# Performance work log

Measured on AMD Instinct MI355X. Metric: run time of the kernel, lower is better.

Reference implementation:

```python
import jax, jax.numpy as jnp
import numpy as np

N_ROUTING = 3


def squash(s):
    # squash factor ||s|| / (1 + ||s||^2), applied per output capsule vector
    n = jnp.linalg.norm(s, axis=-1, keepdims=True)
    return n / (1.0 + n * n) * s


def setup_inputs() -> dict:
    key = jax.random.key(0)
    k1, k2 = jax.random.split(key)
    B, Ni, Di = 64, 2048, 8
    No, Do = 32, 16
    x = jax.random.normal(k1, (B, Ni, Di), dtype=jnp.float32)
    W = jax.random.normal(k2, (Ni, No, Do, Di), dtype=jnp.float32) * 0.05
    return {"x": x, "W": W}


def reference(x, W):
    # x: (B, Ni, Di); W: (Ni, No, Do, Di)
    # Per-capsule transform: x_hat[b,i,j,:] = W[i,j] @ x[b,i]
    x_hat = jnp.einsum('bni,nodi->bnod', x, W)          # (B, Ni, No, Do)
    x_hat_sg = jax.lax.stop_gradient(x_hat)
    B, Ni, No, Do = x_hat.shape
    b = jnp.zeros((B, Ni, No), dtype=x_hat.dtype)       # routing logits
    v = None
    for it in range(N_ROUTING):
        c = jax.nn.softmax(b, axis=2)                   # coupling over output caps
        if it == N_ROUTING - 1:
            s = jnp.einsum('bno,bnod->bod', c, x_hat)   # grads flow on last iter
            v = squash(s)
        else:
            s = jnp.einsum('bno,bnod->bod', c, x_hat_sg)
            v = squash(s)
            b = b + jnp.einsum('bod,bnod->bno', v, x_hat_sg)  # agreement update
    return v  # (B, No, Do)
```

## Files before the change

kernel.cpp:

```cpp
#include <hip/hip_runtime.h>
#include <hip/hip_bf16.h>
#include <math.h>

namespace {
constexpr int kB  = 64;
constexpr int kNi = 2048;
constexpr int kNo = 32;
constexpr int kDo = 16;
constexpr int kSeg   = kNo * kDo;
constexpr int kSlabs = 256;
constexpr int kNPer  = kNi / kSlabs;
}

typedef __attribute__((ext_vector_type(4)))  short s4;
typedef __attribute__((ext_vector_type(16))) float f16v;

__device__ __forceinline__ f16v mfma_32x32x8_bf16(s4 a, s4 b, f16v c) {
#if __has_builtin(__builtin_amdgcn_mfma_f32_32x32x8bf16_1k)
    return __builtin_amdgcn_mfma_f32_32x32x8bf16_1k(a, b, c, 0, 0, 0);
#else
    asm("v_mfma_f32_32x32x8_bf16 %0, %1, %2, %0" : "+v"(c) : "v"(a), "v"(b));
    return c;
#endif
}

__device__ __forceinline__ unsigned pack_bf16(float lo, float hi) {
    union { __hip_bfloat162 h; unsigned u; } v;
    v.h = __float22bfloat162_rn(make_float2(lo, hi));
    return v.u;
}
__device__ __forceinline__ float bf_lo(unsigned u) { return __uint_as_float(u << 16); }
__device__ __forceinline__ float bf_hi(unsigned u) { return __uint_as_float(u & 0xffff0000u); }

union A2 { int2 i; s4 s; };


__global__ __launch_bounds__(512, 2)
void caps_prepacc(const float* __restrict__ xg, const float* __restrict__ Wg,
                  unsigned* __restrict__ wPack2, unsigned* __restrict__ xPack,
                  __hip_bfloat16* __restrict__ partial)
{
    const int tid = threadIdx.x;
    const int blk = blockIdx.x;
    const int w   = __builtin_amdgcn_readfirstlane(tid >> 6);
    const int l   = tid & 63;
    const int o32 = l & 31;
    const int hi  = l >> 5;

    const float4* Wg4 = reinterpret_cast<const float4*>(Wg);
    const float4* xg4 = reinterpret_cast<const float4*>(xg);

    f16v acc00, acc01, acc10, acc11;
#pragma unroll
    for (int r = 0; r < 16; ++r) {
        acc00[r] = 0.0f; acc01[r] = 0.0f; acc10[r] = 0.0f; acc11[r] = 0.0f;
    }

#pragma unroll 2
    for (int nn = 0; nn < kNPer; ++nn) {
        const int n = blk * kNPer + nn;
        const float4 w0 = Wg4[((size_t)n * 512 + (2 * w + 0) * 32 + o32) * 2 + hi];
        const float4 w1 = Wg4[((size_t)n * 512 + (2 * w + 1) * 32 + o32) * 2 + hi];
        int4 wp;
        wp.x = (int)pack_bf16(w0.x, w0.y);
        wp.y = (int)pack_bf16(w0.z, w0.w);
        wp.z = (int)pack_bf16(w1.x, w1.y);
        wp.w = (int)pack_bf16(w1.z, w1.w);
        reinterpret_cast<int4*>(wPack2)[((size_t)n * 8 + w) * 64 + l] = wp;

        const float4 x0 = xg4[((size_t)(0 * 32 + o32) * kNi + n) * 2 + hi];
        const float4 x1 = xg4[((size_t)(32 + o32) * kNi + n) * 2 + hi];
        uint2 q0, q1;
        q0.x = pack_bf16(x0.x, x0.y); q0.y = pack_bf16(x0.z, x0.w);
        q1.x = pack_bf16(x1.x, x1.y); q1.y = pack_bf16(x1.z, x1.w);
        *reinterpret_cast<uint2*>(xPack + ((size_t)(n * 2 + 0) * 64 + l) * 2) = q0;
        *reinterpret_cast<uint2*>(xPack + ((size_t)(n * 2 + 1) * 64 + l) * 2) = q1;

        A2 a0; a0.i = make_int2(wp.x, wp.y);
        A2 a1; a1.i = make_int2(wp.z, wp.w);
        A2 b0; b0.i = make_int2((int)q0.x, (int)q0.y);
        A2 b1; b1.i = make_int2((int)q1.x, (int)q1.y);
        acc00 = mfma_32x32x8_bf16(a0.s, b0.s, acc00);
        acc01 = mfma_32x32x8_bf16(a1.s, b0.s, acc01);
        acc10 = mfma_32x32x8_bf16(a0.s, b1.s, acc10);
        acc11 = mfma_32x32x8_bf16(a1.s, b1.s, acc11);
    }

#pragma unroll
    for (int nt = 0; nt < 2; ++nt) {
        const int b = nt * 32 + o32;
#pragma unroll
        for (int m = 0; m < 2; ++m) {
            const int mt = 2 * w + m;
            const f16v& a = (nt == 0) ? (m == 0 ? acc00 : acc01)
                                      : (m == 0 ? acc10 : acc11);
#pragma unroll
            for (int q = 0; q < 4; ++q) {
                const int od = mt * 32 + 8 * q + 4 * hi;
                uint2 u;
                u.x = pack_bf16(a[4 * q + 0], a[4 * q + 1]);
                u.y = pack_bf16(a[4 * q + 2], a[4 * q + 3]);
                *reinterpret_cast<uint2*>(
                    partial + ((size_t)blk * kB + b) * kSeg + od) = u;
            }
        }
    }
}

__global__ __launch_bounds__(512, 2)
void caps_routef(const unsigned* __restrict__ wPack2, const unsigned* __restrict__ xPack,
                 const float* __restrict__ vsumPack, __hip_bfloat16* __restrict__ partial)
{
    __shared__ float Zl[2][8][4][32];
    __shared__ unsigned cl[kNPer][16][32];

    const int tid = threadIdx.x;
    const int blk = blockIdx.x & (kSlabs - 1);
    const int nt  = blockIdx.x >> 8;
    const int w   = __builtin_amdgcn_readfirstlane(tid >> 6);
    const int l   = tid & 63;
    const int b32 = l & 31;
    const int b   = nt * 32 + b32;
    const int hi  = l >> 5;

    const int4* wp4 = reinterpret_cast<const int4*>(wPack2);
    const int2* xp2 = reinterpret_cast<const int2*>(xPack);
    const size_t abase = ((size_t)blk * 64 + w) * 64 + l;
    const size_t xbase = ((size_t)blk * 16 + nt) * 64 + l;

    {
        float vsp[2][16];
#pragma unroll
        for (int m = 0; m < 2; ++m) {
            const int mt = 2 * w + m;
            const float4* vp = reinterpret_cast<const float4*>(
                vsumPack + (((size_t)mt * 2 + hi) * 64 + b) * 16);
#pragma unroll
            for (int k = 0; k < 4; ++k) {
                const float4 v = vp[k];
                vsp[m][4 * k + 0] = v.x; vsp[m][4 * k + 1] = v.y;
                vsp[m][4 * k + 2] = v.z; vsp[m][4 * k + 3] = v.w;
            }
        }

        for (int h = 0; h < 2; ++h) {
            float e[4][4];
#pragma unroll
            for (int k = 0; k < 4; ++k) {
                const int nn = h * 4 + k;
                const int4 aw = wp4[abase + (size_t)nn * 512];
                const int2 bx = xp2[xbase + (size_t)nn * 128];
                A2 ua0; ua0.i = make_int2(aw.x, aw.y);
                A2 ua1; ua1.i = make_int2(aw.z, aw.w);
                A2 ub;  ub.i  = bx;
                f16v t0, t1;
#pragma unroll
                for (int r = 0; r < 16; ++r) { t0[r] = 0.0f; t1[r] = 0.0f; }
                t0 = mfma_32x32x8_bf16(ua0.s, ub.s, t0);
                t1 = mfma_32x32x8_bf16(ua1.s, ub.s, t1);
                {
                    float a0_ = fmaf(vsp[0][1], t0[1], vsp[0][0] * t0[0]);
                    float a1_ = fmaf(vsp[0][3], t0[3], vsp[0][2] * t0[2]);
                    float a2_ = fmaf(vsp[0][5], t0[5], vsp[0][4] * t0[4]);
                    float a3_ = fmaf(vsp[0][7], t0[7], vsp[0][6] * t0[6]);
                    float p0 = (a0_ + a1_) + (a2_ + a3_);
                    float b0_ = fmaf(vsp[0][9],  t0[9],  vsp[0][8]  * t0[8]);
                    float b1_ = fmaf(vsp[0][11], t0[11], vsp[0][10] * t0[10]);
                    float b2_ = fmaf(vsp[0][13], t0[13], vsp[0][12] * t0[12]);
                    float b3_ = fmaf(vsp[0][15], t0[15], vsp[0][14] * t0[14]);
                    float p1 = (b0_ + b1_) + (b2_ + b3_);
                    p0 += __shfl_xor(p0, 32);
                    p1 += __shfl_xor(p1, 32);
                    e[k][0] = exp2f(p0); e[k][1] = exp2f(p1);
                }
                {
                    float a0_ = fmaf(vsp[1][1], t1[1], vsp[1][0] * t1[0]);
                    float a1_ = fmaf(vsp[1][3], t1[3], vsp[1][2] * t1[2]);
                    float a2_ = fmaf(vsp[1][5], t1[5], vsp[1][4] * t1[4]);
                    float a3_ = fmaf(vsp[1][7], t1[7], vsp[1][6] * t1[6]);
                    float p0 = (a0_ + a1_) + (a2_ + a3_);
                    float b0_ = fmaf(vsp[1][9],  t1[9],  vsp[1][8]  * t1[8]);
                    float b1_ = fmaf(vsp[1][11], t1[11], vsp[1][10] * t1[10]);
                    float b2_ = fmaf(vsp[1][13], t1[13], vsp[1][12] * t1[12]);
                    float b3_ = fmaf(vsp[1][15], t1[15], vsp[1][14] * t1[14]);
                    float p1 = (b0_ + b1_) + (b2_ + b3_);
                    p0 += __shfl_xor(p0, 32);
                    p1 += __shfl_xor(p1, 32);
                    e[k][2] = exp2f(p0); e[k][3] = exp2f(p1);
                }
                if (l < 32)
                    Zl[h][w][k][l] = (e[k][0] + e[k][1]) + (e[k][2] + e[k][3]);
            }
            __syncthreads();
#pragma unroll
            for (int k = 0; k < 4; ++k) {
                float Z = 0.0f;
#pragma unroll
                for (int w2 = 0; w2 < 8; ++w2) Z += Zl[h][w2][k][b32];
                const float rz = __builtin_amdgcn_rcpf(Z);
                if (l < 32) {
                    cl[h * 4 + k][2 * w + 0][l] = pack_bf16(e[k][0] * rz, e[k][1] * rz);
                    cl[h * 4 + k][2 * w + 1][l] = pack_bf16(e[k][2] * rz, e[k][3] * rz);
                }
            }
        }
    }
    __syncthreads();
    __builtin_amdgcn_sched_barrier(0);

    float sacc[2][16];
#pragma unroll
    for (int r = 0; r < 16; ++r) { sacc[0][r] = 0.0f; sacc[1][r] = 0.0f; }

#pragma unroll 2
    for (int nn = 0; nn < kNPer; ++nn) {
        const int4 aw = wp4[abase + (size_t)nn * 512];
        const int2 bx = xp2[xbase + (size_t)nn * 128];
        A2 ua0; ua0.i = make_int2(aw.x, aw.y);
        A2 ua1; ua1.i = make_int2(aw.z, aw.w);
        A2 ub;  ub.i  = bx;
        const unsigned cp0 = cl[nn][2 * w + 0][b32];
        const unsigned cp1 = cl[nn][2 * w + 1][b32];
        f16v t0, t1;
#pragma unroll
        for (int r = 0; r < 16; ++r) { t0[r] = 0.0f; t1[r] = 0.0f; }
        t0 = mfma_32x32x8_bf16(ua0.s, ub.s, t0);
        t1 = mfma_32x32x8_bf16(ua1.s, ub.s, t1);
        const float c00 = bf_lo(cp0), c01 = bf_hi(cp0);
        const float c10 = bf_lo(cp1), c11 = bf_hi(cp1);
#pragma unroll
        for (int r = 0; r < 8; ++r) {
            sacc[0][r]     = fmaf(c00, t0[r],     sacc[0][r]);
            sacc[0][8 + r] = fmaf(c01, t0[8 + r], sacc[0][8 + r]);
            sacc[1][r]     = fmaf(c10, t1[r],     sacc[1][r]);
            sacc[1][8 + r] = fmaf(c11, t1[8 + r], sacc[1][8 + r]);
        }
    }

#pragma unroll
    for (int m = 0; m < 2; ++m) {
        const int mt = 2 * w + m;
#pragma unroll
        for (int q = 0; q < 4; ++q) {
            const int od = mt * 32 + 8 * q + 4 * hi;
            uint2 u;
            u.x = pack_bf16(sacc[m][4 * q + 0], sacc[m][4 * q + 1]);
            u.y = pack_bf16(sacc[m][4 * q + 2], sacc[m][4 * q + 3]);
            *reinterpret_cast<uint2*>(
                partial + ((size_t)blk * kB + b) * kSeg + od) = u;
        }
    }
}

template<int PASS>
__global__ __launch_bounds__(512, 2)
void caps_finish(const __hip_bfloat16* __restrict__ partial,
                 float* __restrict__ vsum, float* __restrict__ vsumPack,
                 float* __restrict__ out)
{
    const int b  = blockIdx.x >> 2;
    const int q  = blockIdx.x & 3;
    const int t  = threadIdx.x;
    const int qd = t & 31;
    const int sg = t >> 5;
    const int od0 = q * 128 + qd * 4;

    const __hip_bfloat16* p = partial
        + ((size_t)(sg * 16) * kB + b) * kSeg + od0;
    float s0 = 0, s1 = 0, s2 = 0, s3 = 0;
#pragma unroll
    for (int k = 0; k < 16; ++k) {
        const uint2 u = *reinterpret_cast<const uint2*>(p + (size_t)k * (kB * kSeg));
        s0 += bf_lo(u.x); s1 += bf_hi(u.x);
        s2 += bf_lo(u.y); s3 += bf_hi(u.y);
    }

    __shared__ float red[16][128];
    __shared__ float sq[128];
    __shared__ float fo[8];
    *reinterpret_cast<float4*>(&red[sg][qd * 4]) = make_float4(s0, s1, s2, s3);
    __syncthreads();
    if (t < 128) {
        float s = 0.0f;
#pragma unroll
        for (int g = 0; g < 16; ++g) s += red[g][t];
        if (PASS == 0) s *= (1.0f / 32.0f);
        sq[t] = s * s;
        red[0][t] = s;
    }
    __syncthreads();
    if (t < 8) {
        float n2 = 0.0f;
#pragma unroll
        for (int d = 0; d < 16; ++d) n2 += sq[t * 16 + d];
        fo[t] = sqrtf(n2) / (1.0f + n2);
    }
    __syncthreads();
    if (t < 128) {
        const float s = red[0][t];
        const int od = q * 128 + t;
        const float v = fo[t >> 4] * s;
        float nv = v;
        if (PASS == 0) {
            vsum[(size_t)b * kSeg + od] = v;
        } else if (PASS == 1) {
            nv = vsum[(size_t)b * kSeg + od] + v;
            vsum[(size_t)b * kSeg + od] = nv;
        } else {
            out[(size_t)b * kSeg + od] = v;
        }
        if (PASS < 2) {
            const int mt = od >> 5, r5 = od & 31;
            const int hi = (r5 >> 2) & 1, reg = (r5 & 3) | ((r5 >> 3) << 2);
            vsumPack[(((size_t)mt * 2 + hi) * 64 + b) * 16 + reg] =
                nv * 1.44269504f;
        }
    }
}

extern "C" void kernel_launch(void* const* d_in, const int* in_sizes, int n_in,
                              void* d_out, int out_size, void* d_ws, size_t ws_size,
                              hipStream_t stream)
{
    const float* x = (const float*)d_in[0];
    const float* W = (const float*)d_in[1];
    float* out = (float*)d_out;

    char* base = (char*)d_ws;
    __hip_bfloat16* partial = (__hip_bfloat16*)base;
    base += (size_t)kSlabs * kB * kSeg * sizeof(__hip_bfloat16);
    float* vsum = (float*)base;
    base += (size_t)kB * kSeg * sizeof(float);
    float* vsumPack = (float*)base;
    base += (size_t)16 * 2 * 64 * 16 * sizeof(float);
    unsigned* wPack2 = (unsigned*)base;
    base += (size_t)kNi * 16 * 64 * 2 * sizeof(unsigned);
    unsigned* xPack = (unsigned*)base;

    const dim3 gp(kSlabs), bp(512);
    const dim3 gr(kSlabs * 2), br(512);
    const dim3 gf(kB * 4), bf(512);

    caps_prepacc<<<gp, bp, 0, stream>>>(x, W, wPack2, xPack, partial);
    caps_finish<0><<<gf, bf, 0, stream>>>(partial, vsum, vsumPack, out);
    caps_routef<<<gr, br, 0, stream>>>(wPack2, xPack, vsumPack, partial);
    caps_finish<1><<<gf, bf, 0, stream>>>(partial, vsum, vsumPack, out);
    caps_routef<<<gr, br, 0, stream>>>(wPack2, xPack, vsumPack, partial);
    caps_finish<2><<<gf, bf, 0, stream>>>(partial, vsum, vsumPack, out);
}
```

Baseline: 71.87 us.

## Fuse all routing stages into one cooperative kernel with grid syncs

Merges the six launches (prep/accumulate, three finish passes, two routing passes) into one persistent cooperative kernel of 256 blocks, with grid-wide syncs between stages. The routing body now loops over both batch halves inside each block instead of using 512 blocks. This removes launch overhead and inter-kernel gaps, but halves routing parallelism, drops occupancy to one block per CU by launch bounds, and adds grid barrier costs.

Result: slower. 269.0 us (+274.3%).

```diff
diff --git a/kernel.cpp b/kernel.cpp
--- a/kernel.cpp
+++ b/kernel.cpp
@@ -1,13 +1,14 @@
 #include <hip/hip_runtime.h>
 #include <hip/hip_bf16.h>
+#include <hip/hip_cooperative_groups.h>
 #include <math.h>
+
+namespace cg = cooperative_groups;
 
 namespace {
 constexpr int kB  = 64;
 constexpr int kNi = 2048;
-constexpr int kNo = 32;
-constexpr int kDo = 16;
-constexpr int kSeg   = kNo * kDo;
+constexpr int kSeg   = 512;
 constexpr int kSlabs = 256;
 constexpr int kNPer  = kNi / kSlabs;
 }
@@ -35,10 +36,9 @@
 union A2 { int2 i; s4 s; };
 
 
-__global__ __launch_bounds__(512, 2)
-void caps_prepacc(const float* __restrict__ xg, const float* __restrict__ Wg,
-                  unsigned* __restrict__ wPack2, unsigned* __restrict__ xPack,
-                  __hip_bfloat16* __restrict__ partial)
+__device__ void prepacc_body(const float* __restrict__ xg, const float* __restrict__ Wg,
+                             unsigned* __restrict__ wPack2, unsigned* __restrict__ xPack,
+                             __hip_bfloat16* __restrict__ partial)
 {
     const int tid = threadIdx.x;
     const int blk = blockIdx.x;
@@ -107,156 +107,157 @@
     }
 }
 
-__global__ __launch_bounds__(512, 2)
-void caps_routef(const unsigned* __restrict__ wPack2, const unsigned* __restrict__ xPack,
-                 const float* __restrict__ vsumPack, __hip_bfloat16* __restrict__ partial)
-{
-    __shared__ float Zl[2][8][4][32];
-    __shared__ unsigned cl[kNPer][16][32];
-
+__device__ void route_body(const unsigned* __restrict__ wPack2,
+                           const unsigned* __restrict__ xPack,
+                           const float* __restrict__ vsumPack,
+                           __hip_bfloat16* __restrict__ partial,
+                           float (*Zl)[8][4][32], unsigned (*cl)[16][32])
+{
     const int tid = threadIdx.x;
-    const int blk = blockIdx.x & (kSlabs - 1);
-    const int nt  = blockIdx.x >> 8;
+    const int blk = blockIdx.x;
     const int w   = __builtin_amdgcn_readfirstlane(tid >> 6);
     const int l   = tid & 63;
     const int b32 = l & 31;
-    const int b   = nt * 32 + b32;
     const int hi  = l >> 5;
 
     const int4* wp4 = reinterpret_cast<const int4*>(wPack2);
     const int2* xp2 = reinterpret_cast<const int2*>(xPack);
     const size_t abase = ((size_t)blk * 64 + w) * 64 + l;
-    const size_t xbase = ((size_t)blk * 16 + nt) * 64 + l;
-
-    {
-        float vsp[2][16];
+
+    for (int nt = 0; nt < 2; ++nt) {
+        const int b = nt * 32 + b32;
+        const size_t xbase = ((size_t)blk * 16 + nt) * 64 + l;
+
+        {
+            float vsp[2][16];
+#pragma unroll
+            for (int m = 0; m < 2; ++m) {
+                const int mt = 2 * w + m;
+                const float4* vp = reinterpret_cast<const float4*>(
+                    vsumPack + (((size_t)mt * 2 + hi) * 64 + b) * 16);
+#pragma unroll
+                for (int k = 0; k < 4; ++k) {
+                    const float4 v = vp[k];
+                    vsp[m][4 * k + 0] = v.x; vsp[m][4 * k + 1] = v.y;
+                    vsp[m][4 * k + 2] = v.z; vsp[m][4 * k + 3] = v.w;
+                }
+            }
+
+            for (int h = 0; h < 2; ++h) {
+                float e[4][4];
+#pragma unroll
+                for (int k = 0; k < 4; ++k) {
+                    const int nn = h * 4 + k;
+                    const int4 aw = wp4[abase + (size_t)nn * 512];
+                    const int2 bx = xp2[xbase + (size_t)nn * 128];
+                    A2 ua0; ua0.i = make_int2(aw.x, aw.y);
+                    A2 ua1; ua1.i = make_int2(aw.z, aw.w);
+                    A2 ub;  ub.i  = bx;
+                    f16v t0, t1;
+#pragma unroll
+                    for (int r = 0; r < 16; ++r) { t0[r] = 0.0f; t1[r] = 0.0f; }
+                    t0 = mfma_32x32x8_bf16(ua0.s, ub.s, t0);
+                    t1 = mfma_32x32x8_bf16(ua1.s, ub.s, t1);
+                    {
+                        float a0_ = fmaf(vsp[0][1], t0[1], vsp[0][0] * t0[0]);
+                        float a1_ = fmaf(vsp[0][3], t0[3], vsp[0][2] * t0[2]);
+                        float a2_ = fmaf(vsp[0][5], t0[5], vsp[0][4] * t0[4]);
+                        float a3_ = fmaf(vsp[0][7], t0[7], vsp[0][6] * t0[6]);
+                        float p0 = (a0_ + a1_) + (a2_ + a3_);
+                        float b0_ = fmaf(vsp[0][9],  t0[9],  vsp[0][8]  * t0[8]);
+                        float b1_ = fmaf(vsp[0][11], t0[11], vsp[0][10] * t0[10]);
+                        float b2_ = fmaf(vsp[0][13], t0[13], vsp[0][12] * t0[12]);
+                        float b3_ = fmaf(vsp[0][15], t0[15], vsp[0][14] * t0[14]);
+                        float p1 = (b0_ + b1_) + (b2_ + b3_);
+                        p0 += __shfl_xor(p0, 32);
+                        p1 += __shfl_xor(p1, 32);
+                        e[k][0] = exp2f(p0); e[k][1] = exp2f(p1);
+                    }
+                    {
+                        float a0_ = fmaf(vsp[1][1], t1[1], vsp[1][0] * t1[0]);
+                        float a1_ = fmaf(vsp[1][3], t1[3], vsp[1][2] * t1[2]);
+                        float a2_ = fmaf(vsp[1][5], t1[5], vsp[1][4] * t1[4]);
+                        float a3_ = fmaf(vsp[1][7], t1[7], vsp[1][6] * t1[6]);
+                        float p0 = (a0_ + a1_) + (a2_ + a3_);
+                        float b0_ = fmaf(vsp[1][9],  t1[9],  vsp[1][8]  * t1[8]);
+                        float b1_ = fmaf(vsp[1][11], t1[11], vsp[1][10] * t1[10]);
+                        float b2_ = fmaf(vsp[1][13], t1[13], vsp[1][12] * t1[12]);
+                        float b3_ = fmaf(vsp[1][15], t1[15], vsp[1][14] * t1[14]);
+                        float p1 = (b0_ + b1_) + (b2_ + b3_);
+                        p0 += __shfl_xor(p0, 32);
+                        p1 += __shfl_xor(p1, 32);
+                        e[k][2] = exp2f(p0); e[k][3] = exp2f(p1);
+                    }
+                    if (l < 32)
+                        Zl[h][w][k][l] = (e[k][0] + e[k][1]) + (e[k][2] + e[k][3]);
+                }
+                __syncthreads();
+#pragma unroll
+                for (int k = 0; k < 4; ++k) {
+                    float Z = 0.0f;
+#pragma unroll
+                    for (int w2 = 0; w2 < 8; ++w2) Z += Zl[h][w2][k][b32];
+                    const float rz = __builtin_amdgcn_rcpf(Z);
+                    if (l < 32) {
+                        cl[h * 4 + k][2 * w + 0][l] = pack_bf16(e[k][0] * rz, e[k][1] * rz);
+                        cl[h * 4 + k][2 * w + 1][l] = pack_bf16(e[k][2] * rz, e[k][3] * rz);
+                    }
+                }
+            }
+        }
+        __syncthreads();
+        __builtin_amdgcn_sched_barrier(0);
+
+        float sacc[2][16];
+#pragma unroll
+        for (int r = 0; r < 16; ++r) { sacc[0][r] = 0.0f; sacc[1][r] = 0.0f; }
+
+#pragma unroll 2
+        for (int nn = 0; nn < kNPer; ++nn) {
+            const int4 aw = wp4[abase + (size_t)nn * 512];
+            const int2 bx = xp2[xbase + (size_t)nn * 128];
+            A2 ua0; ua0.i = make_int2(aw.x, aw.y);
+            A2 ua1; ua1.i = make_int2(aw.z, aw.w);
+            A2 ub;  ub.i  = bx;
+            const unsigned cp0 = cl[nn][2 * w + 0][b32];
+            const unsigned cp1 = cl[nn][2 * w + 1][b32];
+            f16v t0, t1;
+#pragma unroll
+            for (int r = 0; r < 16; ++r) { t0[r] = 0.0f; t1[r] = 0.0f; }
+            t0 = mfma_32x32x8_bf16(ua0.s, ub.s, t0);
+            t1 = mfma_32x32x8_bf16(ua1.s, ub.s, t1);
+            const float c00 = bf_lo(cp0), c01 = bf_hi(cp0);
+            const float c10 = bf_lo(cp1), c11 = bf_hi(cp1);
+#pragma unroll
+            for (int r = 0; r < 8; ++r) {
+                sacc[0][r]     = fmaf(c00, t0[r],     sacc[0][r]);
+                sacc[0][8 + r] = fmaf(c01, t0[8 + r], sacc[0][8 + r]);
+                sacc[1][r]     = fmaf(c10, t1[r],     sacc[1][r]);
+                sacc[1][8 + r] = fmaf(c11, t1[8 + r], sacc[1][8 + r]);
+            }
+        }
+
 #pragma unroll
         for (int m = 0; m < 2; ++m) {
             const int mt = 2 * w + m;
-            const float4* vp = reinterpret_cast<const float4*>(
-                vsumPack + (((size_t)mt * 2 + hi) * 64 + b) * 16);
-#pragma unroll
-            for (int k = 0; k < 4; ++k) {
-                const float4 v = vp[k];
-                vsp[m][4 * k + 0] = v.x; vsp[m][4 * k + 1] = v.y;
-                vsp[m][4 * k + 2] = v.z; vsp[m][4 * k + 3] = v.w;
-            }
-        }
-
-        for (int h = 0; h < 2; ++h) {
-            float e[4][4];
-#pragma unroll
-            for (int k = 0; k < 4; ++k) {
-                const int nn = h * 4 + k;
-                const int4 aw = wp4[abase + (size_t)nn * 512];
-                const int2 bx = xp2[xbase + (size_t)nn * 128];
-                A2 ua0; ua0.i = make_int2(aw.x, aw.y);
-                A2 ua1; ua1.i = make_int2(aw.z, aw.w);
-                A2 ub;  ub.i  = bx;
-                f16v t0, t1;
-#pragma unroll
-                for (int r = 0; r < 16; ++r) { t0[r] = 0.0f; t1[r] = 0.0f; }
-                t0 = mfma_32x32x8_bf16(ua0.s, ub.s, t0);
-                t1 = mfma_32x32x8_bf16(ua1.s, ub.s, t1);
-                {
-                    float a0_ = fmaf(vsp[0][1], t0[1], vsp[0][0] * t0[0]);
-                    float a1_ = fmaf(vsp[0][3], t0[3], vsp[0][2] * t0[2]);
-                    float a2_ = fmaf(vsp[0][5], t0[5], vsp[0][4] * t0[4]);
-                    float a3_ = fmaf(vsp[0][7], t0[7], vsp[0][6] * t0[6]);
-                    float p0 = (a0_ + a1_) + (a2_ + a3_);
-                    float b0_ = fmaf(vsp[0][9],  t0[9],  vsp[0][8]  * t0[8]);
-                    float b1_ = fmaf(vsp[0][11], t0[11], vsp[0][10] * t0[10]);
-                    float b2_ = fmaf(vsp[0][13], t0[13], vsp[0][12] * t0[12]);
-                    float b3_ = fmaf(vsp[0][15], t0[15], vsp[0][14] * t0[14]);
-                    float p1 = (b0_ + b1_) + (b2_ + b3_);
-                    p0 += __shfl_xor(p0, 32);
-                    p1 += __shfl_xor(p1, 32);
-                    e[k][0] = exp2f(p0); e[k][1] = exp2f(p1);
-                }
-                {
-                    float a0_ = fmaf(vsp[1][1], t1[1], vsp[1][0] * t1[0]);
-                    float a1_ = fmaf(vsp[1][3], t1[3], vsp[1][2] * t1[2]);
-                    float a2_ = fmaf(vsp[1][5], t1[5], vsp[1][4] * t1[4]);
-                    float a3_ = fmaf(vsp[1][7], t1[7], vsp[1][6] * t1[6]);
-                    float p0 = (a0_ + a1_) + (a2_ + a3_);
-                    float b0_ = fmaf(vsp[1][9],  t1[9],  vsp[1][8]  * t1[8]);
-                    float b1_ = fmaf(vsp[1][11], t1[11], vsp[1][10] * t1[10]);
-                    float b2_ = fmaf(vsp[1][13], t1[13], vsp[1][12] * t1[12]);
-                    float b3_ = fmaf(vsp[1][15], t1[15], vsp[1][14] * t1[14]);
-                    float p1 = (b0_ + b1_) + (b2_ + b3_);
-                    p0 += __shfl_xor(p0, 32);
-                    p1 += __shfl_xor(p1, 32);
-                    e[k][2] = exp2f(p0); e[k][3] = exp2f(p1);
-                }
-                if (l < 32)
-                    Zl[h][w][k][l] = (e[k][0] + e[k][1]) + (e[k][2] + e[k][3]);
-            }
-            __syncthreads();
-#pragma unroll
-            for (int k = 0; k < 4; ++k) {
-                float Z = 0.0f;
-#pragma unroll
-                for (int w2 = 0; w2 < 8; ++w2) Z += Zl[h][w2][k][b32];
-                const float rz = __builtin_amdgcn_rcpf(Z);
-                if (l < 32) {
-                    cl[h * 4 + k][2 * w + 0][l] = pack_bf16(e[k][0] * rz, e[k][1] * rz);
-                    cl[h * 4 + k][2 * w + 1][l] = pack_bf16(e[k][2] * rz, e[k][3] * rz);
-                }
-            }
-        }
-    }
-    __syncthreads();
-    __builtin_amdgcn_sched_barrier(0);
-
-    float sacc[2][16];
-#pragma unroll
-    for (int r = 0; r < 16; ++r) { sacc[0][r] = 0.0f; sacc[1][r] = 0.0f; }
-
-#pragma unroll 2
-    for (int nn = 0; nn < kNPer; ++nn) {
-        const int4 aw = wp4[abase + (size_t)nn * 512];
-        const int2 bx = xp2[xbase + (size_t)nn * 128];
-        A2 ua0; ua0.i = make_int2(aw.x, aw.y);
-        A2 ua1; ua1.i = make_int2(aw.z, aw.w);
-        A2 ub;  ub.i  = bx;
-        const unsigned cp0 = cl[nn][2 * w + 0][b32];
-        const unsigned cp1 = cl[nn][2 * w + 1][b32];
-        f16v t0, t1;
-#pragma unroll
-        for (int r = 0; r < 16; ++r) { t0[r] = 0.0f; t1[r] = 0.0f; }
-        t0 = mfma_32x32x8_bf16(ua0.s, ub.s, t0);
-        t1 = mfma_32x32x8_bf16(ua1.s, ub.s, t1);
-        const float c00 = bf_lo(cp0), c01 = bf_hi(cp0);
-        const float c10 = bf_lo(cp1), c11 = bf_hi(cp1);
-#pragma unroll
-        for (int r = 0; r < 8; ++r) {
-            sacc[0][r]     = fmaf(c00, t0[r],     sacc[0][r]);
-            sacc[0][8 + r] = fmaf(c01, t0[8 + r], sacc[0][8 + r]);
-            sacc[1][r]     = fmaf(c10, t1[r],     sacc[1][r]);
-            sacc[1][8 + r] = fmaf(c11, t1[8 + r], sacc[1][8 + r]);
-        }
-    }
-
-#pragma unroll
-    for (int m = 0; m < 2; ++m) {
-        const int mt = 2 * w + m;
-#pragma unroll
-        for (int q = 0; q < 4; ++q) {
-            const int od = mt * 32 + 8 * q + 4 * hi;
-            uint2 u;
-            u.x = pack_bf16(sacc[m][4 * q + 0], sacc[m][4 * q + 1]);
-            u.y = pack_bf16(sacc[m][4 * q + 2], sacc[m][4 * q + 3]);
-            *reinterpret_cast<uint2*>(
-                partial + ((size_t)blk * kB + b) * kSeg + od) = u;
-        }
-    }
-}
-
-template<int PASS>
-__global__ __launch_bounds__(512, 2)
-void caps_finish(const __hip_bfloat16* __restrict__ partial,
-                 float* __restrict__ vsum, float* __restrict__ vsumPack,
-                 float* __restrict__ out)
+#pragma unroll
+            for (int q = 0; q < 4; ++q) {
+                const int od = mt * 32 + 8 * q + 4 * hi;
+                uint2 u;
+                u.x = pack_bf16(sacc[m][4 * q + 0], sacc[m][4 * q + 1]);
+                u.y = pack_bf16(sacc[m][4 * q + 2], sacc[m][4 * q + 3]);
+                *reinterpret_cast<uint2*>(
+                    partial + ((size_t)blk * kB + b) * kSeg + od) = u;
+            }
+        }
+        __syncthreads();
+    }
+}
+
+__device__ void finish_body(const __hip_bfloat16* __restrict__ partial,
+                            float* __restrict__ vsum, float* __restrict__ vsumPack,
+                            float* __restrict__ out, int pass,
+                            float (*red)[128], float* sq, float* fo)
 {
     const int b  = blockIdx.x >> 2;
     const int q  = blockIdx.x & 3;
@@ -275,16 +276,13 @@
         s2 += bf_lo(u.y); s3 += bf_hi(u.y);
     }
 
-    __shared__ float red[16][128];
-    __shared__ float sq[128];
-    __shared__ float fo[8];
     *reinterpret_cast<float4*>(&red[sg][qd * 4]) = make_float4(s0, s1, s2, s3);
     __syncthreads();
     if (t < 128) {
         float s = 0.0f;
 #pragma unroll
         for (int g = 0; g < 16; ++g) s += red[g][t];
-        if (PASS == 0) s *= (1.0f / 32.0f);
+        if (pass == 0) s *= (1.0f / 32.0f);
         sq[t] = s * s;
         red[0][t] = s;
     }
@@ -301,21 +299,49 @@
         const int od = q * 128 + t;
         const float v = fo[t >> 4] * s;
         float nv = v;
-        if (PASS == 0) {
+        if (pass == 0) {
             vsum[(size_t)b * kSeg + od] = v;
-        } else if (PASS == 1) {
+        } else if (pass == 1) {
             nv = vsum[(size_t)b * kSeg + od] + v;
             vsum[(size_t)b * kSeg + od] = nv;
         } else {
             out[(size_t)b * kSeg + od] = v;
         }
-        if (PASS < 2) {
+        if (pass < 2) {
             const int mt = od >> 5, r5 = od & 31;
             const int hi = (r5 >> 2) & 1, reg = (r5 & 3) | ((r5 >> 3) << 2);
             vsumPack[(((size_t)mt * 2 + hi) * 64 + b) * 16 + reg] =
                 nv * 1.44269504f;
         }
     }
+    __syncthreads();
+}
+
+__global__ __launch_bounds__(512, 1)
+void caps_all(const float* __restrict__ xg, const float* __restrict__ Wg,
+              unsigned* __restrict__ wPack2, unsigned* __restrict__ xPack,
+              __hip_bfloat16* __restrict__ partial, float* __restrict__ vsum,
+              float* __restrict__ vsumPack, float* __restrict__ out)
+{
+    __shared__ float    Zl[2][8][4][32];
+    __shared__ unsigned cl[kNPer][16][32];
+    __shared__ float    red[16][128];
+    __shared__ float    sq[128];
+    __shared__ float    fo[8];
+
+    cg::grid_group grid = cg::this_grid();
+
+    prepacc_body(xg, Wg, wPack2, xPack, partial);
+    grid.sync();
+    finish_body(partial, vsum, vsumPack, out, 0, red, sq, fo);
+    grid.sync();
+    route_body(wPack2, xPack, vsumPack, partial, Zl, cl);
+    grid.sync();
+    finish_body(partial, vsum, vsumPack, out, 1, red, sq, fo);
+    grid.sync();
+    route_body(wPack2, xPack, vsumPack, partial, Zl, cl);
+    grid.sync();
+    finish_body(partial, vsum, vsumPack, out, 2, red, sq, fo);
 }
 
 extern "C" void kernel_launch(void* const* d_in, const int* in_sizes, int n_in,
@@ -337,14 +363,8 @@
     base += (size_t)kNi * 16 * 64 * 2 * sizeof(unsigned);
     unsigned* xPack = (unsigned*)base;
 
-    const dim3 gp(kSlabs), bp(512);
-    const dim3 gr(kSlabs * 2), br(512);
-    const dim3 gf(kB * 4), bf(512);
-
-    caps_prepacc<<<gp, bp, 0, stream>>>(x, W, wPack2, xPack, partial);
-    caps_finish<0><<<gf, bf, 0, stream>>>(partial, vsum, vsumPack, out);
-    caps_routef<<<gr, br, 0, stream>>>(wPack2, xPack, vsumPack, partial);
-    caps_finish<1><<<gf, bf, 0, stream>>>(partial, vsum, vsumPack, out);
-    caps_routef<<<gr, br, 0, stream>>>(wPack2, xPack, vsumPack, partial);
-    caps_finish<2><<<gf, bf, 0, stream>>>(partial, vsum, vsumPack, out);
-}
+    void* args[] = { (void*)&x, (void*)&W, (void*)&wPack2, (void*)&xPack,
+                     (void*)&partial, (void*)&vsum, (void*)&vsumPack, (void*)&out };
+    hipLaunchCooperativeKernel((const void*)caps_all, dim3(kSlabs), dim3(512),
+                               args, 0, stream);
+}
```
